# Kernel optimization log

Hardware: AMD Instinct MI355X
Metric: run time of the kernel (lower is better)

The kernel has to match this reference:

```python
import jax, jax.numpy as jnp
import numpy as np

ALPHA, GAMMA = 0.25, 2.0
W_CLS, W_REG, W_DIR = 1.0, 2.0, 0.2
X_MIN, X_MAX = 0.0, 200.0
Y_MIN, Y_MAX = -50.0, 50.0
SX = 0.2 * 2  # voxel_size_x * backbone_stride
SY = 0.2 * 2
IGNORE_R = 1
CLS_CH = 0  # anchor_id*num_classes + car_class_id


def _bce_logits(x, t):
    # numerically stable BCE-with-logits, matches F.binary_cross_entropy_with_logits
    return jnp.maximum(x, 0.0) - x * t + jnp.log1p(jnp.exp(-jnp.abs(x)))


def _build_targets(gt_boxes, B, H, W):
    # gt_boxes: [B, N, 8] = (x, y, z, l, w, h, rot, cls_id)
    x, y, z, l, w_, h, rot, cid = [gt_boxes[..., i] for i in range(8)]
    valid = (cid == 0.0) & (x >= X_MIN) & (x < X_MAX) & (y >= Y_MIN) & (y < Y_MAX)
    gx = jnp.floor((x - X_MIN) / SX).astype(jnp.int32)
    gy = jnp.floor((y - Y_MIN) / SY).astype(jnp.int32)
    valid &= (gx >= 0) & (gx < W) & (gy >= 0) & (gy < H)

    bidx = jnp.broadcast_to(jnp.arange(B)[:, None], x.shape)
    BHW = B * H * W
    flat = (bidx * H + gy) * W + gx                      # [B, N]
    flat = jnp.where(valid, flat, BHW).reshape(-1)        # sentinel -> dropped scatter

    cls_t = jnp.zeros((BHW,), jnp.float32).at[flat].set(1.0, mode='drop')

    cell_cx = X_MIN + (gx.astype(jnp.float32) + 0.5) * SX
    cell_cy = Y_MIN + (gy.astype(jnp.float32) + 0.5) * SY
    dx = (x - cell_cx) / SX
    dy = (y - cell_cy) / SY
    vals = jnp.stack([dx, dy, z,
                      jnp.log(jnp.maximum(l, 1e-3)),
                      jnp.log(jnp.maximum(w_, 1e-3)),
                      jnp.log(jnp.maximum(h, 1e-3)),
                      jnp.sin(rot)], axis=0).reshape(7, -1)   # [7, B*N]
    reg_t = jnp.zeros((7, BHW), jnp.float32).at[:, flat].set(vals, mode='drop')

    dir_bin = jnp.where(jnp.cos(rot) >= 0.0, 0, 1).reshape(-1)
    dir_t = jnp.zeros((2, BHW), jnp.float32).at[dir_bin, flat].set(1.0, mode='drop')

    pos = jnp.zeros((BHW,), bool).at[flat].set(True, mode='drop')  # reg_mask == dir_mask

    # ignore-radius window around each positive on the car cls channel
    ign = jnp.zeros((BHW,), bool)
    gxf, gyf, bf, vf = gx.reshape(-1), gy.reshape(-1), bidx.reshape(-1), valid.reshape(-1)
    for oy in range(-IGNORE_R, IGNORE_R + 1):
        for ox in range(-IGNORE_R, IGNORE_R + 1):
            gy2, gx2 = gyf + oy, gxf + ox
            ok = vf & (gy2 >= 0) & (gy2 < H) & (gx2 >= 0) & (gx2 < W)
            f2 = jnp.where(ok, (bf * H + gy2) * W + gx2, BHW)
            ign = ign.at[f2].set(True, mode='drop')
    cls_valid_ch = (~ign) | pos  # box centers always stay valid

    return (cls_t.reshape(B, H, W), reg_t.reshape(7, B, H, W),
            dir_t.reshape(2, B, H, W), cls_valid_ch.reshape(B, H, W),
            pos.reshape(B, H, W))


def reference(cls_pred, reg_pred, dir_pred, gt_boxes, batch_size):
    B, _, H, W = cls_pred.shape
    cls_t1, reg_t, dir_t, cls_valid1, pos = _build_targets(gt_boxes, B, H, W)

    cls_target = jnp.zeros_like(cls_pred).at[:, CLS_CH].set(cls_t1)
    cls_valid = jnp.ones(cls_pred.shape, bool).at[:, CLS_CH].set(cls_valid1)
    reg_target = jnp.moveaxis(reg_t, 1, 0)  # [B, 7, H, W]
    dir_target = jnp.moveaxis(dir_t, 1, 0)  # [B, 2, H, W]

    # focal loss, masked
    p = jax.nn.sigmoid(cls_pred)
    bce = _bce_logits(cls_pred, cls_target)
    p_t = p * cls_target + (1.0 - p) * (1.0 - cls_target)
    a_t = ALPHA * cls_target + (1.0 - ALPHA) * (1.0 - cls_target)
    vm = cls_valid.astype(cls_pred.dtype)
    cls_loss = jnp.sum(a_t * (1.0 - p_t) ** GAMMA * bce * vm) / jnp.maximum(vm.sum(), 1.0)

    # smooth L1 on positive cells (mean over 7*npos masked elements)
    posf = pos[:, None].astype(reg_pred.dtype)  # [B, 1, H, W]
    d = jnp.abs(reg_pred - reg_target)
    sl1 = jnp.where(d < 1.0, 0.5 * d * d, d - 0.5)
    n_reg = posf.sum() * 7.0
    reg_loss = jnp.sum(sl1 * posf) / jnp.maximum(n_reg, 1.0)

    # direction BCE on positive cells (mean over 2*npos masked elements)
    dbce = _bce_logits(dir_pred, dir_target)
    n_dir = posf.sum() * 2.0
    dir_loss = jnp.sum(dbce * posf) / jnp.maximum(n_dir, 1.0)

    total = W_CLS * cls_loss + W_REG * reg_loss + W_DIR * dir_loss
    return total, cls_loss, reg_loss, dir_loss


def setup_inputs() -> dict:
    key = jax.random.key(0)
    ks = jax.random.split(key, 11)
    B, H, W, N = 16, 250, 500, 64
    cls_pred = jax.random.normal(ks[0], (B, 3, H, W), jnp.float32)
    reg_pred = jax.random.normal(ks[1], (B, 7, H, W), jnp.float32)
    dir_pred = jax.random.normal(ks[2], (B, 2, H, W), jnp.float32)
    x = jax.random.uniform(ks[3], (B, N)) * 210.0 - 5.0
    y = jax.random.uniform(ks[4], (B, N)) * 110.0 - 55.0
    z = jax.random.uniform(ks[5], (B, N)) * 3.0 - 1.5
    l = jax.random.uniform(ks[6], (B, N)) * 2.0 + 3.0
    w = jax.random.uniform(ks[7], (B, N)) * 0.7 + 1.5
    h = jax.random.uniform(ks[8], (B, N)) * 0.8 + 1.2
    rot = jax.random.uniform(ks[9], (B, N)) * (2.0 * np.pi) - np.pi
    cid = jax.random.randint(ks[10], (B, N), 0, 3).astype(jnp.float32)
    gt_boxes = jnp.stack([x, y, z, l, w, h, rot, cid], axis=-1)
    return {"cls_pred": cls_pred, "reg_pred": reg_pred, "dir_pred": dir_pred,
            "gt_boxes": gt_boxes, "batch_size": B}
```

## Files before the change

kernel.cpp:

```cpp
#include <hip/hip_runtime.h>


#define B_   16
#define NC_  3
#define H_   250
#define W_   500
#define N_   64
#define HW_  125000
#define TOTAL_CLS 6000000
#define N4   1500000
#define THREADS 256
#define DENSE_BLOCKS 1024
#define GRID (B_ + DENSE_BLOCKS)

#define HSLOTS 1024
#define ILIST  576

#define CLS_OFF 64
#define CNT_IDX 2048

#define PUB_F(p, v) __hip_atomic_store((p), (v), __ATOMIC_RELAXED, __HIP_MEMORY_SCOPE_AGENT)
#define PUB_U(p, v) __hip_atomic_store((p), (v), __ATOMIC_RELAXED, __HIP_MEMORY_SCOPE_AGENT)
#define RD_F(p)     __hip_atomic_load((p), __ATOMIC_RELAXED, __HIP_MEMORY_SCOPE_AGENT)
#define RD_U(p)     __hip_atomic_load((p), __ATOMIC_RELAXED, __HIP_MEMORY_SCOPE_AGENT)

__device__ __forceinline__ void sig_bce0(float x, float& p, float& bce0) {
    float ax = fabsf(x);
    float em = __expf(-ax);
    float lg = __logf(1.0f + em);
    bce0 = fmaxf(x, 0.0f) + lg;
    float r1 = __fdividef(1.0f, 1.0f + em);
    p = (x >= 0.0f) ? r1 : em * r1;
}
__device__ __forceinline__ float focal0(float x) {
    float p, b; sig_bce0(x, p, b);
    return 0.75f * p * p * b;
}
__device__ __forceinline__ float focal_delta(float x) {
    float p, b; sig_bce0(x, p, b);
    float q = 1.0f - p;
    return 0.25f * q * q * (b - x) - 0.75f * p * p * b;
}

__global__ __launch_bounds__(THREADS) void main_kernel(
        const float* __restrict__ cls, const float* __restrict__ reg,
        const float* __restrict__ dirp, const float* __restrict__ gt,
        float* __restrict__ fws, float* __restrict__ out) {
    __shared__ unsigned s_hash[HSLOTS];
    __shared__ unsigned s_list[ILIST];
    __shared__ unsigned s_pospix[N_];
    __shared__ unsigned s_cnt[2];
    __shared__ float    s_acc[3];
    __shared__ unsigned s_uacc;
    __shared__ float    sw[4];
    __shared__ int      s_last;
    const int tid = threadIdx.x;
    unsigned* uws = (unsigned*)fws;

    if (blockIdx.x >= B_) {
        const int gbid = blockIdx.x - B_;
        const float4* c4 = (const float4*)cls;
        float s0 = 0.f, s1 = 0.f, s2 = 0.f, s3 = 0.f;
        const int stride = DENSE_BLOCKS * THREADS;
        for (int k = gbid * THREADS + tid; k < N4; k += stride) {
            float4 v = c4[k];
            s0 += focal0(v.x); s1 += focal0(v.y);
            s2 += focal0(v.z); s3 += focal0(v.w);
        }
        float sum = (s0 + s1) + (s2 + s3);
        #pragma unroll
        for (int off = 32; off > 0; off >>= 1) sum += __shfl_down(sum, off, 64);
        if ((tid & 63) == 0) sw[tid >> 6] = sum;
        __syncthreads();
        if (tid == 0)
            PUB_F(&fws[CLS_OFF + blockIdx.x], (sw[0] + sw[1]) + (sw[2] + sw[3]));
    } else {
        const int b = blockIdx.x;
        for (int i = tid; i < HSLOTS; i += THREADS) s_hash[i] = 0xFFFFFFFFu;
        if (tid < 2) s_cnt[tid] = 0u;
        if (tid < 3) s_acc[tid] = 0.f;
        if (tid == 0) s_uacc = 0u;
        __syncthreads();

        float my_reg = 0.f, my_dir = 0.f, my_corr = 0.f;
        unsigned my_cign = 0u;

        if (tid < 64) {
            const float4* g4 = (const float4*)(gt + (b * N_ + tid) * 8);
            float4 p0 = g4[0], p1 = g4[1];
            float x = p0.x, y = p0.y, z = p0.z, l = p0.w;
            float wb = p1.x, h = p1.y, rot = p1.z, cid = p1.w;
            bool valid = (cid == 0.0f) && (x >= 0.0f) && (x < 200.0f) &&
                         (y >= -50.0f) && (y < 50.0f);
            int gx = 0, gy = 0;
            if (valid) {
                gx = (int)floorf(x / 0.4f);
                gy = (int)floorf((y + 50.0f) / 0.4f);
                valid = (gx >= 0) && (gx < W_) && (gy >= 0) && (gy < H_);
            }
            const int pix = gy * W_ + gx;
            const unsigned bin = (cosf(rot) >= 0.0f) ? 1u : 2u;

            unsigned long long vm = __ballot(valid);
            int last = -1; unsigned ub = 0u;
            for (int l2 = 0; l2 < 64; ++l2) {
                int p2 = __shfl(pix, l2, 64);
                unsigned b2 = __shfl(bin, l2, 64);
                if (valid && ((vm >> l2) & 1ull) && p2 == pix) { last = l2; ub |= b2; }
            }
            bool winner = valid && (last == tid);
            if (winner) s_pospix[atomicAdd(&s_cnt[1], 1u)] = (unsigned)pix;

            if (valid) {
                for (int oy = -1; oy <= 1; ++oy) {
                    int gy2 = gy + oy; if (gy2 < 0 || gy2 >= H_) continue;
                    for (int ox = -1; ox <= 1; ++ox) {
                        int gx2 = gx + ox; if (gx2 < 0 || gx2 >= W_) continue;
                        unsigned cell = (unsigned)(gy2 * W_ + gx2);
                        unsigned hh = (cell * 2654435761u) >> 22;
                        for (;;) {
                            unsigned old = atomicCAS(&s_hash[hh], 0xFFFFFFFFu, cell);
                            if (old == 0xFFFFFFFFu) {
                                s_list[atomicAdd(&s_cnt[0], 1u)] = cell;
                                break;
                            }
                            if (old == cell) break;
                            hh = (hh + 1u) & (HSLOTS - 1u);
                        }
                    }
                }
            }

            if (winner) {
                float cx = ((float)gx + 0.5f) * 0.4f;
                float cy = -50.0f + ((float)gy + 0.5f) * 0.4f;
                float tgt[7] = {(x - cx) / 0.4f, (y - cy) / 0.4f, z,
                                logf(fmaxf(l, 1e-3f)), logf(fmaxf(wb, 1e-3f)),
                                logf(fmaxf(h, 1e-3f)), sinf(rot)};
                #pragma unroll
                for (int c = 0; c < 7; ++c) {
                    float d = fabsf(reg[(b * 7 + c) * HW_ + pix] - tgt[c]);
                    my_reg += (d < 1.0f) ? 0.5f * d * d : d - 0.5f;
                }
                #pragma unroll
                for (int c = 0; c < 2; ++c) {
                    float xd = dirp[(b * 2 + c) * HW_ + pix];
                    float t = (float)((ub >> c) & 1u);
                    my_dir += fmaxf(xd, 0.0f) - xd * t +
                              __logf(1.0f + __expf(-fabsf(xd)));
                }
                my_corr += focal_delta(cls[(b * NC_) * HW_ + pix]);
            }
        }
        __syncthreads();

        {
            const float* cls0 = cls + (b * NC_) * HW_;
            const unsigned icnt = s_cnt[0], pcnt = s_cnt[1];
            for (unsigned i = tid; i < icnt; i += THREADS) {
                unsigned cell = s_list[i];
                bool isp = false;
                for (unsigned j = 0; j < pcnt; ++j) isp |= (s_pospix[j] == cell);
                if (!isp) { my_corr -= focal0(cls0[cell]); my_cign++; }
            }
        }
        #pragma unroll
        for (int off = 32; off > 0; off >>= 1) {
            my_corr += __shfl_down(my_corr, off, 64);
            my_reg  += __shfl_down(my_reg,  off, 64);
            my_dir  += __shfl_down(my_dir,  off, 64);
            my_cign += __shfl_down(my_cign, off, 64);
        }
        if ((tid & 63) == 0) {
            atomicAdd(&s_acc[0], my_corr);
            atomicAdd(&s_acc[1], my_reg);
            atomicAdd(&s_acc[2], my_dir);
            atomicAdd(&s_uacc, my_cign);
        }
        __syncthreads();
        if (tid == 0) {
            PUB_F(&fws[b],      s_acc[1]);
            PUB_F(&fws[16 + b], s_acc[2]);
            PUB_U(&uws[32 + b], s_uacc);
            PUB_U(&uws[48 + b], s_cnt[1]);
            PUB_F(&fws[CLS_OFF + b], s_acc[0]);
        }
    }

    if (tid == 0) {
        asm volatile("s_waitcnt vmcnt(0)" ::: "memory");
        unsigned old = __hip_atomic_fetch_add(&uws[CNT_IDX], 1u,
                           __ATOMIC_RELAXED, __HIP_MEMORY_SCOPE_AGENT);
        s_last = (old == 0xAAAAAAAAu + (unsigned)(GRID - 1)) ||
                 (old == (unsigned)(GRID - 1));
    }
    __syncthreads();
    if (s_last) {
        __builtin_amdgcn_fence(__ATOMIC_ACQUIRE, "agent");
        float cs = 0.f;
        for (int k = tid; k < GRID; k += THREADS)
            cs += RD_F(&fws[CLS_OFF + k]);
        float rs = 0.f, ds = 0.f, ic = 0.f, np = 0.f;
        if (tid < B_) {
            rs = RD_F(&fws[tid]);
            ds = RD_F(&fws[16 + tid]);
            ic = (float)RD_U(&uws[32 + tid]);
            np = (float)RD_U(&uws[48 + tid]);
        }
        #pragma unroll
        for (int off = 32; off > 0; off >>= 1) {
            cs += __shfl_down(cs, off, 64);
            rs += __shfl_down(rs, off, 64);
            ds += __shfl_down(ds, off, 64);
            ic += __shfl_down(ic, off, 64);
            np += __shfl_down(np, off, 64);
        }
        if ((tid & 63) == 0) sw[tid >> 6] = cs;
        __syncthreads();
        if (tid == 0) {
            float cst = (sw[0] + sw[1]) + (sw[2] + sw[3]);
            float vm = (float)TOTAL_CLS - ic;
            float cls_loss = cst / fmaxf(vm, 1.0f);
            float reg_loss = rs / fmaxf(np * 7.0f, 1.0f);
            float dir_loss = ds / fmaxf(np * 2.0f, 1.0f);
            out[0] = cls_loss + 2.0f * reg_loss + 0.2f * dir_loss;
            out[1] = cls_loss;
            out[2] = reg_loss;
            out[3] = dir_loss;
        }
    }
}

extern "C" void kernel_launch(void* const* d_in, const int* in_sizes, int n_in,
                              void* d_out, int out_size, void* d_ws, size_t ws_size,
                              hipStream_t stream) {
    const float* cls_pred = (const float*)d_in[0];
    const float* reg_pred = (const float*)d_in[1];
    const float* dir_pred = (const float*)d_in[2];
    const float* gt_boxes = (const float*)d_in[3];
    float* fws = (float*)d_ws;
    float* out = (float*)d_out;

    main_kernel<<<GRID, THREADS, 0, stream>>>(cls_pred, reg_pred, dir_pred,
                                              gt_boxes, fws, out);
}
```

Baseline: 123.1 us.

## Use 1024-thread blocks and global atomic accumulation for loss reduction

Raises the block size from 256 to 1024 threads, which cuts the dense focal-loss grid to 240 blocks and gives each per-batch block four times the threads for its target-building work. Per-block partial results are no longer stored to separate workspace slots and re-reduced by the last block. Every block now atomically adds into five global accumulators, and the last block only reads those and subtracts the assumed poison value. This removes the final multi-slot reduction at the cost of contended atomics, and it depends on the workspace starting at either zero or the 0xAA poison pattern.

```diff
diff --git a/kernel.cpp b/kernel.cpp
--- a/kernel.cpp
+++ b/kernel.cpp
@@ -9,20 +9,16 @@
 #define HW_  125000
 #define TOTAL_CLS 6000000
 #define N4   1500000
-#define THREADS 256
-#define DENSE_BLOCKS 1024
+#define THREADS 1024
+#define NWAVES (THREADS / 64)
+#define DENSE_BLOCKS 240
 #define GRID (B_ + DENSE_BLOCKS)
 
 #define HSLOTS 1024
 #define ILIST  576
 
-#define CLS_OFF 64
-#define CNT_IDX 2048
-
-#define PUB_F(p, v) __hip_atomic_store((p), (v), __ATOMIC_RELAXED, __HIP_MEMORY_SCOPE_AGENT)
-#define PUB_U(p, v) __hip_atomic_store((p), (v), __ATOMIC_RELAXED, __HIP_MEMORY_SCOPE_AGENT)
-#define RD_F(p)     __hip_atomic_load((p), __ATOMIC_RELAXED, __HIP_MEMORY_SCOPE_AGENT)
-#define RD_U(p)     __hip_atomic_load((p), __ATOMIC_RELAXED, __HIP_MEMORY_SCOPE_AGENT)
+#define CNT_IDX 64
+#define POISON_U 0xAAAAAAAAu
 
 __device__ __forceinline__ void sig_bce0(float x, float& p, float& bce0) {
     float ax = fabsf(x);
@@ -50,10 +46,10 @@
     __shared__ unsigned s_list[ILIST];
     __shared__ unsigned s_pospix[N_];
     __shared__ unsigned s_cnt[2];
-    __shared__ float    s_acc[3];
-    __shared__ unsigned s_uacc;
-    __shared__ float    sw[4];
-    __shared__ int      s_last;
+    __shared__ float    sw[NWAVES];
+    __shared__ float    sw2[NWAVES], sw3[NWAVES];
+    __shared__ unsigned swu[NWAVES];
+    __shared__ int      s_last, s_zero;
     const int tid = threadIdx.x;
     unsigned* uws = (unsigned*)fws;
 
@@ -72,14 +68,16 @@
         for (int off = 32; off > 0; off >>= 1) sum += __shfl_down(sum, off, 64);
         if ((tid & 63) == 0) sw[tid >> 6] = sum;
         __syncthreads();
-        if (tid == 0)
-            PUB_F(&fws[CLS_OFF + blockIdx.x], (sw[0] + sw[1]) + (sw[2] + sw[3]));
+        if (tid == 0) {
+            float t = 0.f;
+            #pragma unroll
+            for (int i = 0; i < NWAVES; ++i) t += sw[i];
+            atomicAdd(&fws[0], t);
+        }
     } else {
         const int b = blockIdx.x;
         for (int i = tid; i < HSLOTS; i += THREADS) s_hash[i] = 0xFFFFFFFFu;
         if (tid < 2) s_cnt[tid] = 0u;
-        if (tid < 3) s_acc[tid] = 0.f;
-        if (tid == 0) s_uacc = 0u;
         __syncthreads();
 
         float my_reg = 0.f, my_dir = 0.f, my_corr = 0.f;
@@ -172,18 +170,21 @@
             my_cign += __shfl_down(my_cign, off, 64);
         }
         if ((tid & 63) == 0) {
-            atomicAdd(&s_acc[0], my_corr);
-            atomicAdd(&s_acc[1], my_reg);
-            atomicAdd(&s_acc[2], my_dir);
-            atomicAdd(&s_uacc, my_cign);
+            int wv = tid >> 6;
+            sw[wv] = my_corr; sw2[wv] = my_reg; sw3[wv] = my_dir; swu[wv] = my_cign;
         }
         __syncthreads();
         if (tid == 0) {
-            PUB_F(&fws[b],      s_acc[1]);
-            PUB_F(&fws[16 + b], s_acc[2]);
-            PUB_U(&uws[32 + b], s_uacc);
-            PUB_U(&uws[48 + b], s_cnt[1]);
-            PUB_F(&fws[CLS_OFF + b], s_acc[0]);
+            float tc = 0.f, tr = 0.f, td = 0.f; unsigned tu = 0u;
+            #pragma unroll
+            for (int i = 0; i < NWAVES; ++i) {
+                tc += sw[i]; tr += sw2[i]; td += sw3[i]; tu += swu[i];
+            }
+            atomicAdd(&fws[0], tc);
+            atomicAdd(&fws[1], tr);
+            atomicAdd(&fws[2], td);
+            atomicAdd(&uws[3], tu);
+            atomicAdd(&uws[4], s_cnt[1]);
         }
     }
 
@@ -191,43 +192,34 @@
         asm volatile("s_waitcnt vmcnt(0)" ::: "memory");
         unsigned old = __hip_atomic_fetch_add(&uws[CNT_IDX], 1u,
                            __ATOMIC_RELAXED, __HIP_MEMORY_SCOPE_AGENT);
-        s_last = (old == 0xAAAAAAAAu + (unsigned)(GRID - 1)) ||
+        s_last = (old == POISON_U + (unsigned)(GRID - 1)) ||
                  (old == (unsigned)(GRID - 1));
+        s_zero = (old == (unsigned)(GRID - 1));
     }
     __syncthreads();
-    if (s_last) {
+    if (s_last && tid == 0) {
         __builtin_amdgcn_fence(__ATOMIC_ACQUIRE, "agent");
-        float cs = 0.f;
-        for (int k = tid; k < GRID; k += THREADS)
-            cs += RD_F(&fws[CLS_OFF + k]);
-        float rs = 0.f, ds = 0.f, ic = 0.f, np = 0.f;
-        if (tid < B_) {
-            rs = RD_F(&fws[tid]);
-            ds = RD_F(&fws[16 + tid]);
-            ic = (float)RD_U(&uws[32 + tid]);
-            np = (float)RD_U(&uws[48 + tid]);
-        }
-        #pragma unroll
-        for (int off = 32; off > 0; off >>= 1) {
-            cs += __shfl_down(cs, off, 64);
-            rs += __shfl_down(rs, off, 64);
-            ds += __shfl_down(ds, off, 64);
-            ic += __shfl_down(ic, off, 64);
-            np += __shfl_down(np, off, 64);
-        }
-        if ((tid & 63) == 0) sw[tid >> 6] = cs;
-        __syncthreads();
-        if (tid == 0) {
-            float cst = (sw[0] + sw[1]) + (sw[2] + sw[3]);
-            float vm = (float)TOTAL_CLS - ic;
-            float cls_loss = cst / fmaxf(vm, 1.0f);
-            float reg_loss = rs / fmaxf(np * 7.0f, 1.0f);
-            float dir_loss = ds / fmaxf(np * 2.0f, 1.0f);
-            out[0] = cls_loss + 2.0f * reg_loss + 0.2f * dir_loss;
-            out[1] = cls_loss;
-            out[2] = reg_loss;
-            out[3] = dir_loss;
-        }
+        float pf  = s_zero ? 0.0f : __uint_as_float(POISON_U);
+        unsigned pu = s_zero ? 0u : POISON_U;
+        float cs = __hip_atomic_load(&fws[0], __ATOMIC_RELAXED,
+                                     __HIP_MEMORY_SCOPE_AGENT) - pf;
+        float rs = __hip_atomic_load(&fws[1], __ATOMIC_RELAXED,
+                                     __HIP_MEMORY_SCOPE_AGENT) - pf;
+        float ds = __hip_atomic_load(&fws[2], __ATOMIC_RELAXED,
+                                     __HIP_MEMORY_SCOPE_AGENT) - pf;
+        unsigned icu = __hip_atomic_load(&uws[3], __ATOMIC_RELAXED,
+                                     __HIP_MEMORY_SCOPE_AGENT) - pu;
+        unsigned npu = __hip_atomic_load(&uws[4], __ATOMIC_RELAXED,
+                                     __HIP_MEMORY_SCOPE_AGENT) - pu;
+        float ic = (float)icu, np = (float)npu;
+        float vm = (float)TOTAL_CLS - ic;
+        float cls_loss = cs / fmaxf(vm, 1.0f);
+        float reg_loss = rs / fmaxf(np * 7.0f, 1.0f);
+        float dir_loss = ds / fmaxf(np * 2.0f, 1.0f);
+        out[0] = cls_loss + 2.0f * reg_loss + 0.2f * dir_loss;
+        out[1] = cls_loss;
+        out[2] = reg_loss;
+        out[3] = dir_loss;
     }
 }
 
```

After: 118.1 us. 1.04x faster.
